# Optimization experiments

Hardware: AMD Instinct MI355X
Metric: run time of the kernel (lower is better)

## Reference

```python
import jax, jax.numpy as jnp
import numpy as np

I_DECAY = 0.95
STAG_THRESH = 0.95
MAX_GATE = 0.6
MIN_I_GATE = 0.25
EPS = 1e-12


def setup_inputs() -> dict:
    key = jax.random.key(0)
    ks = jax.random.split(key, 9)
    B, T, D_IN, D_OUT = 4, 2048, 2048, 2048
    x = jax.random.normal(ks[0], (B, T, D_IN), dtype=jnp.float32)
    s = 1.0 / np.sqrt(D_IN)
    Wp = jax.random.uniform(ks[1], (D_IN, D_OUT), jnp.float32, -s, s)
    Wi = jax.random.uniform(ks[2], (D_IN, D_OUT), jnp.float32, -s, s) * 0.3
    Wd = jax.random.uniform(ks[3], (D_IN, D_OUT), jnp.float32, -s, s) * 0.3
    gate_w = jax.random.uniform(ks[4], (D_IN, 3), jnp.float32, -s, s)
    gate_b = jnp.array([0.5, 0.0, 0.0], dtype=jnp.float32)
    kick_vec = jax.random.normal(ks[5], (D_OUT,), dtype=jnp.float32) * 0.01
    kick_w = jax.random.uniform(ks[6], (D_IN, 1), jnp.float32, -s, s)
    kick_b = jnp.full((1,), -2.0, dtype=jnp.float32)
    bias = jnp.zeros((D_OUT,), dtype=jnp.float32)
    return {"x": x, "Wp": Wp, "Wi": Wi, "Wd": Wd, "gate_w": gate_w,
            "gate_b": gate_b, "kick_vec": kick_vec, "kick_w": kick_w,
            "kick_b": kick_b, "bias": bias}


def _ema_integral(x, decay):
    # x: [B,T,D] -> time-major scan; integral[0] = x[0]
    xt = jnp.swapaxes(x, 0, 1)  # [T,B,D]

    def step(carry, xcur):
        new = decay * carry + (1.0 - decay) * xcur
        return new, new

    init = xt[0]
    _, rest = jax.lax.scan(step, init, xt[1:])
    integral = jnp.concatenate([init[None], rest], axis=0)
    return jnp.swapaxes(integral, 0, 1)  # [B,T,D]


def reference(x, Wp, Wi, Wd, gate_w, gate_b, kick_vec, kick_w, kick_b, bias):
    B, T, D = x.shape
    # --- EMA integral (linear recurrence over T) ---
    integral = _ema_integral(x, I_DECAY)

    # --- stagnation-aware derivative ---
    diff = jnp.concatenate(
        [jnp.zeros_like(x[:, :1]), x[:, 1:] - x[:, :-1]], axis=1)
    x_norm = x / jnp.maximum(
        jnp.linalg.norm(x, axis=-1, keepdims=True), EPS)
    cos_sim = jnp.concatenate(
        [jnp.zeros((B, 1), x.dtype),
         jnp.sum(x_norm[:, 1:] * x_norm[:, :-1], axis=-1)], axis=1)  # [B,T]
    stagnation = (cos_sim > STAG_THRESH).astype(x.dtype)
    kick_strength = jax.nn.sigmoid(
        jnp.einsum('btd,do->bto', x, kick_w) + kick_b)[..., 0]  # [B,T]
    derivative = diff + (stagnation * kick_strength)[..., None] * kick_vec

    # --- gates: softmax -> clamp max -> clamp I min -> renormalize ---
    g = jax.nn.softmax(jnp.einsum('btd,dg->btg', x, gate_w) + gate_b, axis=-1)
    g = jnp.minimum(g, MAX_GATE)
    g = g.at[..., 1].set(jnp.maximum(g[..., 1], MIN_I_GATE))
    g = g / jnp.sum(g, axis=-1, keepdims=True)

    out = (g[..., 0:1] * jnp.einsum('btd,do->bto', x, Wp)
           + g[..., 1:2] * jnp.einsum('btd,do->bto', integral, Wi)
           + g[..., 2:3] * jnp.einsum('btd,do->bto', derivative, Wd))
    return out + bias
```

## Files before the change

### kernel.cpp

```cpp
#include <hip/hip_runtime.h>

#define DH 2048
#define TT 2048
#define BB 4
#define MROWS 8192
#define KTOT 6144
#define NCH 64
#define LCH 32
#define POW95_L 0.193711483f

typedef __attribute__((ext_vector_type(8))) short bf16x8;
typedef __attribute__((ext_vector_type(4))) float f32x4;

__device__ __forceinline__ unsigned short f2bf(float f) {
  union { float f; unsigned int u; } v; v.f = f;
  unsigned int u = v.u;
  return (unsigned short)((u + 0x7FFFu + ((u >> 16) & 1u)) >> 16);
}

__device__ __forceinline__ void gld16(const unsigned short* g, unsigned short* l) {
  __builtin_amdgcn_global_load_lds((const __attribute__((address_space(1))) void*)g,
                                   (__attribute__((address_space(3))) void*)l, 16, 0, 0);
}

__global__ __launch_bounds__(256) void prep_w(const float* __restrict__ Wp,
                                              const float* __restrict__ Wi,
                                              const float* __restrict__ Wd,
                                              unsigned short* __restrict__ Wt) {
  __shared__ float tile[64][65];
  int bid = blockIdx.x;
  int mat = bid >> 10;
  int t2 = bid & 1023;
  int dt = (t2 >> 5) * 64;
  int ot = (t2 & 31) * 64;
  const float* W = (mat == 0) ? Wp : ((mat == 1) ? Wi : Wd);
  int kbase = mat * DH;
  int tid = threadIdx.x;
  int r = tid >> 4;
  int c4 = (tid & 15) * 4;
#pragma unroll
  for (int i = 0; i < 4; ++i) {
    int rr = r + i * 16;
    float4 v = *(const float4*)&W[(size_t)(dt + rr) * DH + ot + c4];
    tile[rr][c4 + 0] = v.x; tile[rr][c4 + 1] = v.y;
    tile[rr][c4 + 2] = v.z; tile[rr][c4 + 3] = v.w;
  }
  __syncthreads();
  int o = tid >> 3;
  int d8 = (tid & 7) * 8;
#pragma unroll
  for (int pass = 0; pass < 2; ++pass) {
    int oo = o + pass * 32;
    union { unsigned short u[8]; uint4 v; } pk;
#pragma unroll
    for (int i = 0; i < 8; ++i) pk.u[i] = f2bf(tile[d8 + i][oo]);
    *(uint4*)&Wt[(size_t)(ot + oo) * KTOT + kbase + dt + d8] = pk.v;
  }
}

__global__ __launch_bounds__(256) void kv_part_kernel(const float* __restrict__ kick_vec,
                                                      const float* __restrict__ Wd,
                                                      float* __restrict__ part) {
  int blk = blockIdx.x;
  int dchunk = blk >> 3;
  int o = (blk & 7) * 256 + threadIdx.x;
  int d0 = dchunk * 128;
  float s = 0.f;
  for (int i = 0; i < 128; ++i) {
    int d = d0 + i;
    s += kick_vec[d] * Wd[(size_t)d * DH + o];
  }
  part[(size_t)dchunk * DH + o] = s;
}

__global__ __launch_bounds__(256) void kv_reduce_kernel(const float* __restrict__ part,
                                                        float* __restrict__ kvWd) {
  int o = blockIdx.x * 256 + threadIdx.x;
  float s = 0.f;
#pragma unroll
  for (int i = 0; i < 16; ++i) s += part[(size_t)i * DH + o];
  kvWd[o] = s;
}

__global__ __launch_bounds__(256) void rowstats_kernel(const float* __restrict__ x,
                                                       const float* __restrict__ gate_w,
                                                       const float* __restrict__ gate_b,
                                                       const float* __restrict__ kick_w,
                                                       const float* __restrict__ kick_b,
                                                       float* __restrict__ rs) {
  int r = blockIdx.x;
  int t = r & (TT - 1);
  const float* xr = x + (size_t)r * DH;
  const float* xq = xr - DH;
  const bool hp = (t != 0);
  int tid = threadIdx.x;
  float a0 = 0, a1 = 0, a2 = 0, ak = 0, axx = 0, apx = 0, app = 0;
#pragma unroll
  for (int it = 0; it < 2; ++it) {
    int d0 = (tid + it * 256) * 4;
    float4 xv = *(const float4*)(xr + d0);
    float4 pv = hp ? *(const float4*)(xq + d0) : make_float4(0.f, 0.f, 0.f, 0.f);
    float4 q0 = *(const float4*)(gate_w + (size_t)d0 * 3);
    float4 q1 = *(const float4*)(gate_w + (size_t)d0 * 3 + 4);
    float4 q2 = *(const float4*)(gate_w + (size_t)d0 * 3 + 8);
    float4 kw = *(const float4*)(kick_w + d0);
    float xa[4] = {xv.x, xv.y, xv.z, xv.w};
    float pa[4] = {pv.x, pv.y, pv.z, pv.w};
    a0 += xa[0] * q0.x + xa[1] * q0.w + xa[2] * q1.z + xa[3] * q2.y;
    a1 += xa[0] * q0.y + xa[1] * q1.x + xa[2] * q1.w + xa[3] * q2.z;
    a2 += xa[0] * q0.z + xa[1] * q1.y + xa[2] * q2.x + xa[3] * q2.w;
    ak += xa[0] * kw.x + xa[1] * kw.y + xa[2] * kw.z + xa[3] * kw.w;
#pragma unroll
    for (int j = 0; j < 4; ++j) {
      axx += xa[j] * xa[j];
      apx += xa[j] * pa[j];
      app += pa[j] * pa[j];
    }
  }
#pragma unroll
  for (int off = 32; off > 0; off >>= 1) {
    a0 += __shfl_xor(a0, off); a1 += __shfl_xor(a1, off);
    a2 += __shfl_xor(a2, off); ak += __shfl_xor(ak, off);
    axx += __shfl_xor(axx, off); apx += __shfl_xor(apx, off);
    app += __shfl_xor(app, off);
  }
  __shared__ float red[4][7];
  int wv = tid >> 6;
  if ((tid & 63) == 0) {
    red[wv][0] = a0; red[wv][1] = a1; red[wv][2] = a2; red[wv][3] = ak;
    red[wv][4] = axx; red[wv][5] = apx; red[wv][6] = app;
  }
  __syncthreads();
  if (tid == 0) {
    float v[7];
#pragma unroll
    for (int i = 0; i < 7; ++i) v[i] = red[0][i] + red[1][i] + red[2][i] + red[3][i];
    float l0 = v[0] + gate_b[0], l1 = v[1] + gate_b[1], l2 = v[2] + gate_b[2];
    float mx = fmaxf(l0, fmaxf(l1, l2));
    float e0 = expf(l0 - mx), e1 = expf(l1 - mx), e2 = expf(l2 - mx);
    float inv = 1.f / (e0 + e1 + e2);
    float G0 = fminf(e0 * inv, 0.6f);
    float G1 = fminf(e1 * inv, 0.6f);
    float G2 = fminf(e2 * inv, 0.6f);
    G1 = fmaxf(G1, 0.25f);
    float inv2 = 1.f / (G0 + G1 + G2);
    G0 *= inv2; G1 *= inv2; G2 *= inv2;
    float ks = 1.f / (1.f + expf(-(v[3] + kick_b[0])));
    float nn = fmaxf(sqrtf(v[4]), 1e-12f) * fmaxf(sqrtf(v[6]), 1e-12f);
    float cs = hp ? (v[5] / nn) : 0.f;
    float cc = (cs > 0.95f) ? (G2 * ks) : 0.f;
    *(float4*)(rs + (size_t)r * 4) = make_float4(G0, G1, G2, cc);
  }
}

__global__ __launch_bounds__(256) void ema_carry(const float* __restrict__ x,
                                                 float* __restrict__ carry) {
  int gid = blockIdx.x * 256 + threadIdx.x;
  int d = (gid & 511) * 4;
  int ch = (gid >> 9) & (NCH - 1);
  int b = gid >> 15;
  const float* xp = x + ((size_t)b * TT + (size_t)ch * LCH) * DH + d;
  float J0, J1, J2, J3;
  int tstart;
  if (ch == 0) {
    float4 v = *(const float4*)xp;
    J0 = v.x; J1 = v.y; J2 = v.z; J3 = v.w;
    tstart = 1;
  } else {
    J0 = J1 = J2 = J3 = 0.f;
    tstart = 0;
  }
  for (int t = tstart; t < LCH; ++t) {
    float4 v = *(const float4*)(xp + (size_t)t * DH);
    J0 = 0.95f * J0 + 0.05f * v.x;
    J1 = 0.95f * J1 + 0.05f * v.y;
    J2 = 0.95f * J2 + 0.05f * v.z;
    J3 = 0.95f * J3 + 0.05f * v.w;
  }
  *(float4*)&carry[((size_t)b * NCH + ch) * DH + d] = make_float4(J0, J1, J2, J3);
}

__global__ __launch_bounds__(256) void ema_prefix(const float* __restrict__ carry,
                                                  float* __restrict__ P) {
  int gid = blockIdx.x * 256 + threadIdx.x;
  int d = (gid & 511) * 4;
  int b = gid >> 9;
  float4 run = make_float4(0.f, 0.f, 0.f, 0.f);
  for (int ch = 0; ch < NCH; ++ch) {
    size_t idx = ((size_t)b * NCH + ch) * DH + d;
    float4 cv = *(const float4*)&carry[idx];
    *(float4*)&P[idx] = run;
    run.x = cv.x + POW95_L * run.x;
    run.y = cv.y + POW95_L * run.y;
    run.z = cv.z + POW95_L * run.z;
    run.w = cv.w + POW95_L * run.w;
  }
}

__global__ __launch_bounds__(256) void build_a(const float* __restrict__ x,
                                               const float* __restrict__ rs,
                                               const float* __restrict__ P,
                                               unsigned short* __restrict__ A) {
  int gid = blockIdx.x * 256 + threadIdx.x;
  int d = (gid & 255) * 8;
  int ch = (gid >> 8) & (NCH - 1);
  int b = gid >> 14;
  int t0 = ch * LCH;
  const float* xp = x + ((size_t)b * TT + t0) * DH + d;
  unsigned short* Ar = A + ((size_t)b * TT + t0) * KTOT + d;
  float Pv[8], J[8], xprev[8];
  if (ch == 0) {
#pragma unroll
    for (int i = 0; i < 8; ++i) { Pv[i] = 0.f; xprev[i] = 0.f; }
  } else {
    float4 p0 = *(const float4*)&P[((size_t)b * NCH + ch) * DH + d];
    float4 p1 = *(const float4*)&P[((size_t)b * NCH + ch) * DH + d + 4];
    Pv[0] = p0.x; Pv[1] = p0.y; Pv[2] = p0.z; Pv[3] = p0.w;
    Pv[4] = p1.x; Pv[5] = p1.y; Pv[6] = p1.z; Pv[7] = p1.w;
    float4 v0 = *(const float4*)(xp - DH);
    float4 v1 = *(const float4*)(xp - DH + 4);
    xprev[0] = v0.x; xprev[1] = v0.y; xprev[2] = v0.z; xprev[3] = v0.w;
    xprev[4] = v1.x; xprev[5] = v1.y; xprev[6] = v1.z; xprev[7] = v1.w;
  }
#pragma unroll
  for (int i = 0; i < 8; ++i) J[i] = 0.f;
  float f = 1.f;
  const bool first_chunk = (ch == 0);
  for (int tau = 0; tau < LCH; ++tau) {
    float4 v0 = *(const float4*)(xp + (size_t)tau * DH);
    float4 v1 = *(const float4*)(xp + (size_t)tau * DH + 4);
    float xv[8] = {v0.x, v0.y, v0.z, v0.w, v1.x, v1.y, v1.z, v1.w};
    int r = b * TT + t0 + tau;
    float4 g = *(const float4*)&rs[(size_t)r * 4];
    const bool vfirst = first_chunk && (tau == 0);
    f *= 0.95f;
    union { unsigned short u[8]; uint4 v; } op, oi, od;
#pragma unroll
    for (int i = 0; i < 8; ++i) {
      if (vfirst) J[i] = xv[i];
      else J[i] = 0.95f * J[i] + 0.05f * xv[i];
      float I = J[i] + f * Pv[i];
      float diff = vfirst ? 0.f : (xv[i] - xprev[i]);
      op.u[i] = f2bf(g.x * xv[i]);
      oi.u[i] = f2bf(g.y * I);
      od.u[i] = f2bf(g.z * diff);
      xprev[i] = xv[i];
    }
    unsigned short* row = Ar + (size_t)tau * KTOT;
    *(uint4*)(row)          = op.v;
    *(uint4*)(row + DH)     = oi.v;
    *(uint4*)(row + 2 * DH) = od.v;
  }
}

__global__ __launch_bounds__(256) void gemm_kernel(const unsigned short* __restrict__ A,
                                                   const unsigned short* __restrict__ Bt,
                                                   const float* __restrict__ rs,
                                                   const float* __restrict__ kvWd,
                                                   const float* __restrict__ bias,
                                                   float* __restrict__ out) {
  __shared__ __align__(16) unsigned short lA[128 * 64];
  __shared__ __align__(16) unsigned short lB[128 * 64];
  const int tid = threadIdx.x;
  const int wave = tid >> 6, lane = tid & 63;
  const int bid = blockIdx.x;
  const int xcd = bid & 7;
  const int loc = bid >> 3;
  const int mblk = xcd * 8 + (loc & 7);
  const int nblk = loc >> 3;
  const int m0 = mblk * 128, n0 = nblk * 128;

  const int srow = wave * 32 + (lane >> 3);
  const int scol = ((lane & 7) ^ (lane >> 3)) * 8;
  const unsigned short* ga = A + (size_t)(m0 + srow) * KTOT + scol;
  const unsigned short* gb = Bt + (size_t)(n0 + srow) * KTOT + scol;
  unsigned short* la = &lA[(wave * 32) * 64];
  unsigned short* lb = &lB[(wave * 32) * 64];

  f32x4 acc[4][4] = {};
  const int arow = ((wave >> 1) * 64 + (lane & 15)) * 64;
  const int brow = ((wave & 1) * 64 + (lane & 15)) * 64;
  const int cbq = lane >> 4;
  const int swz = lane & 7;

  for (int k0 = 0; k0 < KTOT; k0 += 64) {
#pragma unroll
    for (int j = 0; j < 4; ++j) {
      gld16(ga + k0 + (size_t)j * 8 * KTOT, la + j * 8 * 64);
      gld16(gb + k0 + (size_t)j * 8 * KTOT, lb + j * 8 * 64);
    }
    __syncthreads();
#pragma unroll
    for (int kb = 0; kb < 2; ++kb) {
      const int kphys = ((kb * 4 + cbq) ^ swz) * 8;
      bf16x8 av[4], bv[4];
#pragma unroll
      for (int mi = 0; mi < 4; ++mi)
        av[mi] = *(const bf16x8*)&lA[arow + mi * 16 * 64 + kphys];
#pragma unroll
      for (int ni = 0; ni < 4; ++ni)
        bv[ni] = *(const bf16x8*)&lB[brow + ni * 16 * 64 + kphys];
#pragma unroll
      for (int mi = 0; mi < 4; ++mi)
#pragma unroll
        for (int ni = 0; ni < 4; ++ni)
          acc[mi][ni] = __builtin_amdgcn_mfma_f32_16x16x32_bf16(av[mi], bv[ni], acc[mi][ni], 0, 0, 0);
    }
    __syncthreads();
  }

  const int lr = lane >> 4, lc = lane & 15;
  const int mbase = m0 + (wave >> 1) * 64, nbase = n0 + (wave & 1) * 64;
  float cc[4][4];
#pragma unroll
  for (int mi = 0; mi < 4; ++mi)
#pragma unroll
    for (int rg = 0; rg < 4; ++rg)
      cc[mi][rg] = rs[(size_t)(mbase + mi * 16 + lr * 4 + rg) * 4 + 3];
#pragma unroll
  for (int ni = 0; ni < 4; ++ni) {
    const int n = nbase + ni * 16 + lc;
    const float kv = kvWd[n], bz = bias[n];
#pragma unroll
    for (int mi = 0; mi < 4; ++mi) {
#pragma unroll
      for (int rg = 0; rg < 4; ++rg) {
        const int m = mbase + mi * 16 + lr * 4 + rg;
        out[(size_t)m * DH + n] = acc[mi][ni][rg] + cc[mi][rg] * kv + bz;
      }
    }
  }
}

extern "C" void kernel_launch(void* const* d_in, const int* in_sizes, int n_in,
                              void* d_out, int out_size, void* d_ws, size_t ws_size,
                              hipStream_t stream) {
  const float* x        = (const float*)d_in[0];
  const float* Wp       = (const float*)d_in[1];
  const float* Wi       = (const float*)d_in[2];
  const float* Wd       = (const float*)d_in[3];
  const float* gate_w   = (const float*)d_in[4];
  const float* gate_b   = (const float*)d_in[5];
  const float* kick_vec = (const float*)d_in[6];
  const float* kick_w   = (const float*)d_in[7];
  const float* kick_b   = (const float*)d_in[8];
  const float* bias     = (const float*)d_in[9];
  float* out = (float*)d_out;

  char* ws = (char*)d_ws;
  unsigned short* Wt   = (unsigned short*)(ws + 0);
  unsigned short* Abuf = (unsigned short*)(ws + 25165824);
  float* rs    = (float*)(ws + 125829120);
  float* part  = (float*)(ws + 125960192);
  float* kvWd  = (float*)(ws + 126091264);
  float* carry = (float*)(ws + 126099456);
  float* Pbuf  = (float*)(ws + 128196608);
  (void)ws_size; (void)in_sizes; (void)n_in; (void)out_size;

  prep_w<<<dim3(3072), dim3(256), 0, stream>>>(Wp, Wi, Wd, Wt);
  kv_part_kernel<<<dim3(128), dim3(256), 0, stream>>>(kick_vec, Wd, part);
  kv_reduce_kernel<<<dim3(8), dim3(256), 0, stream>>>(part, kvWd);
  rowstats_kernel<<<dim3(8192), dim3(256), 0, stream>>>(x, gate_w, gate_b, kick_w, kick_b, rs);
  ema_carry<<<dim3(512), dim3(256), 0, stream>>>(x, carry);
  ema_prefix<<<dim3(8), dim3(256), 0, stream>>>(carry, Pbuf);
  build_a<<<dim3(256), dim3(256), 0, stream>>>(x, rs, Pbuf, Abuf);
  gemm_kernel<<<dim3(1024), dim3(256), 0, stream>>>(Abuf, Wt, rs, kvWd, bias, out);
}
```

Before: 444.7 us.

## Fuse kick-vector projection into weight prep and shorten EMA chunks

Computes kick_vec·Wd inside the weight transpose kernel, using the tile already held in shared memory and an atomicAdd after a memset. This removes two separate kernels and a second full pass over Wd. The EMA chunk length is halved to 16 with twice as many chunks, so ema_carry and build_a get more parallelism. build_a also prefetches the next row, is fully unrolled, and reuses the carry buffer in place for the prefix. In exchange, the serial ema_prefix loop gets longer, and the atomics make the kvWd summation order nondeterministic.

```diff
diff --git a/kernel.cpp b/kernel.cpp
--- a/kernel.cpp
+++ b/kernel.cpp
@@ -5,9 +5,9 @@
 #define BB 4
 #define MROWS 8192
 #define KTOT 6144
-#define NCH 64
-#define LCH 32
-#define POW95_L 0.193711483f
+#define NCH 128
+#define LCH 16
+#define POW95_L 0.44012667f
 
 typedef __attribute__((ext_vector_type(8))) short bf16x8;
 typedef __attribute__((ext_vector_type(4))) float f32x4;
@@ -26,7 +26,9 @@
 __global__ __launch_bounds__(256) void prep_w(const float* __restrict__ Wp,
                                               const float* __restrict__ Wi,
                                               const float* __restrict__ Wd,
-                                              unsigned short* __restrict__ Wt) {
+                                              const float* __restrict__ kick_vec,
+                                              unsigned short* __restrict__ Wt,
+                                              float* __restrict__ kvWd) {
   __shared__ float tile[64][65];
   int bid = blockIdx.x;
   int mat = bid >> 10;
@@ -56,30 +58,12 @@
     for (int i = 0; i < 8; ++i) pk.u[i] = f2bf(tile[d8 + i][oo]);
     *(uint4*)&Wt[(size_t)(ot + oo) * KTOT + kbase + dt + d8] = pk.v;
   }
-}
-
-__global__ __launch_bounds__(256) void kv_part_kernel(const float* __restrict__ kick_vec,
-                                                      const float* __restrict__ Wd,
-                                                      float* __restrict__ part) {
-  int blk = blockIdx.x;
-  int dchunk = blk >> 3;
-  int o = (blk & 7) * 256 + threadIdx.x;
-  int d0 = dchunk * 128;
-  float s = 0.f;
-  for (int i = 0; i < 128; ++i) {
-    int d = d0 + i;
-    s += kick_vec[d] * Wd[(size_t)d * DH + o];
-  }
-  part[(size_t)dchunk * DH + o] = s;
-}
-
-__global__ __launch_bounds__(256) void kv_reduce_kernel(const float* __restrict__ part,
-                                                        float* __restrict__ kvWd) {
-  int o = blockIdx.x * 256 + threadIdx.x;
-  float s = 0.f;
-#pragma unroll
-  for (int i = 0; i < 16; ++i) s += part[(size_t)i * DH + o];
-  kvWd[o] = s;
+  if (mat == 2 && tid < 64) {
+    float s = 0.f;
+#pragma unroll 8
+    for (int dd = 0; dd < 64; ++dd) s += kick_vec[dt + dd] * tile[dd][tid];
+    atomicAdd(&kvWd[ot + tid], s);
+  }
 }
 
 __global__ __launch_bounds__(256) void rowstats_kernel(const float* __restrict__ x,
@@ -154,11 +138,11 @@
 }
 
 __global__ __launch_bounds__(256) void ema_carry(const float* __restrict__ x,
-                                                 float* __restrict__ carry) {
+                                                 float* __restrict__ cp) {
   int gid = blockIdx.x * 256 + threadIdx.x;
   int d = (gid & 511) * 4;
   int ch = (gid >> 9) & (NCH - 1);
-  int b = gid >> 15;
+  int b = gid >> 16;
   const float* xp = x + ((size_t)b * TT + (size_t)ch * LCH) * DH + d;
   float J0, J1, J2, J3;
   int tstart;
@@ -170,6 +154,7 @@
     J0 = J1 = J2 = J3 = 0.f;
     tstart = 0;
   }
+#pragma unroll 4
   for (int t = tstart; t < LCH; ++t) {
     float4 v = *(const float4*)(xp + (size_t)t * DH);
     J0 = 0.95f * J0 + 0.05f * v.x;
@@ -177,19 +162,18 @@
     J2 = 0.95f * J2 + 0.05f * v.z;
     J3 = 0.95f * J3 + 0.05f * v.w;
   }
-  *(float4*)&carry[((size_t)b * NCH + ch) * DH + d] = make_float4(J0, J1, J2, J3);
-}
-
-__global__ __launch_bounds__(256) void ema_prefix(const float* __restrict__ carry,
-                                                  float* __restrict__ P) {
+  *(float4*)&cp[((size_t)b * NCH + ch) * DH + d] = make_float4(J0, J1, J2, J3);
+}
+
+__global__ __launch_bounds__(256) void ema_prefix(float* __restrict__ cp) {
   int gid = blockIdx.x * 256 + threadIdx.x;
   int d = (gid & 511) * 4;
   int b = gid >> 9;
   float4 run = make_float4(0.f, 0.f, 0.f, 0.f);
   for (int ch = 0; ch < NCH; ++ch) {
     size_t idx = ((size_t)b * NCH + ch) * DH + d;
-    float4 cv = *(const float4*)&carry[idx];
-    *(float4*)&P[idx] = run;
+    float4 cv = *(const float4*)&cp[idx];
+    *(float4*)&cp[idx] = run;
     run.x = cv.x + POW95_L * run.x;
     run.y = cv.y + POW95_L * run.y;
     run.z = cv.z + POW95_L * run.z;
@@ -201,15 +185,16 @@
                                                const float* __restrict__ rs,
                                                const float* __restrict__ P,
                                                unsigned short* __restrict__ A) {
-  int gid = blockIdx.x * 256 + threadIdx.x;
-  int d = (gid & 255) * 8;
-  int ch = (gid >> 8) & (NCH - 1);
-  int b = gid >> 14;
+  int tid = threadIdx.x;
+  int d = tid * 8;
+  int ch = blockIdx.x & (NCH - 1);
+  int b = blockIdx.x >> 7;
   int t0 = ch * LCH;
   const float* xp = x + ((size_t)b * TT + t0) * DH + d;
   unsigned short* Ar = A + ((size_t)b * TT + t0) * KTOT + d;
   float Pv[8], J[8], xprev[8];
-  if (ch == 0) {
+  const bool first_chunk = (ch == 0);
+  if (first_chunk) {
 #pragma unroll
     for (int i = 0; i < 8; ++i) { Pv[i] = 0.f; xprev[i] = 0.f; }
   } else {
@@ -225,11 +210,16 @@
 #pragma unroll
   for (int i = 0; i < 8; ++i) J[i] = 0.f;
   float f = 1.f;
-  const bool first_chunk = (ch == 0);
+  float4 c0 = *(const float4*)(xp);
+  float4 c1 = *(const float4*)(xp + 4);
+#pragma unroll
   for (int tau = 0; tau < LCH; ++tau) {
-    float4 v0 = *(const float4*)(xp + (size_t)tau * DH);
-    float4 v1 = *(const float4*)(xp + (size_t)tau * DH + 4);
-    float xv[8] = {v0.x, v0.y, v0.z, v0.w, v1.x, v1.y, v1.z, v1.w};
+    float4 n0, n1;
+    if (tau < LCH - 1) {
+      n0 = *(const float4*)(xp + (size_t)(tau + 1) * DH);
+      n1 = *(const float4*)(xp + (size_t)(tau + 1) * DH + 4);
+    }
+    float xv[8] = {c0.x, c0.y, c0.z, c0.w, c1.x, c1.y, c1.z, c1.w};
     int r = b * TT + t0 + tau;
     float4 g = *(const float4*)&rs[(size_t)r * 4];
     const bool vfirst = first_chunk && (tau == 0);
@@ -250,6 +240,7 @@
     *(uint4*)(row)          = op.v;
     *(uint4*)(row + DH)     = oi.v;
     *(uint4*)(row + 2 * DH) = od.v;
+    c0 = n0; c1 = n1;
   }
 }
 
@@ -351,18 +342,15 @@
   unsigned short* Wt   = (unsigned short*)(ws + 0);
   unsigned short* Abuf = (unsigned short*)(ws + 25165824);
   float* rs    = (float*)(ws + 125829120);
-  float* part  = (float*)(ws + 125960192);
-  float* kvWd  = (float*)(ws + 126091264);
-  float* carry = (float*)(ws + 126099456);
-  float* Pbuf  = (float*)(ws + 128196608);
+  float* kvWd  = (float*)(ws + 125960192);
+  float* cp    = (float*)(ws + 125968384);
   (void)ws_size; (void)in_sizes; (void)n_in; (void)out_size;
 
-  prep_w<<<dim3(3072), dim3(256), 0, stream>>>(Wp, Wi, Wd, Wt);
-  kv_part_kernel<<<dim3(128), dim3(256), 0, stream>>>(kick_vec, Wd, part);
-  kv_reduce_kernel<<<dim3(8), dim3(256), 0, stream>>>(part, kvWd);
+  hipMemsetAsync(kvWd, 0, DH * sizeof(float), stream);
+  prep_w<<<dim3(3072), dim3(256), 0, stream>>>(Wp, Wi, Wd, kick_vec, Wt, kvWd);
   rowstats_kernel<<<dim3(8192), dim3(256), 0, stream>>>(x, gate_w, gate_b, kick_w, kick_b, rs);
-  ema_carry<<<dim3(512), dim3(256), 0, stream>>>(x, carry);
-  ema_prefix<<<dim3(8), dim3(256), 0, stream>>>(carry, Pbuf);
-  build_a<<<dim3(256), dim3(256), 0, stream>>>(x, rs, Pbuf, Abuf);
+  ema_carry<<<dim3(1024), dim3(256), 0, stream>>>(x, cp);
+  ema_prefix<<<dim3(8), dim3(256), 0, stream>>>(cp);
+  build_a<<<dim3(512), dim3(256), 0, stream>>>(x, rs, cp, Abuf);
   gemm_kernel<<<dim3(1024), dim3(256), 0, stream>>>(Abuf, Wt, rs, kvWd, bias, out);
 }
```

After: 438.8 us. About the same (-1.3%).
